# Kernel optimization log

Hardware: AMD Instinct MI355X
Metric: run time of the kernel (lower is better)

The kernel has to match this reference:

```python
import jax, jax.numpy as jnp
import numpy as np
from jax import lax

B, T, F, H, V, L = 64, 80, 4096, 512, 32000, 31


def _rn(k, shape, scale=0.05):
    return jax.random.normal(k, shape, dtype=jnp.float32) * scale


def setup_inputs() -> dict:
    key = jax.random.key(0)
    ks = jax.random.split(key, 16)
    emb = _rn(ks[0], (V, H)).at[0].set(0.0)  # padding_idx=0 row zeroed
    return dict(
        video_features=jax.random.normal(ks[1], (B, T, F), jnp.float32),
        captions=jax.random.randint(ks[2], (B, L), 0, V, jnp.int64),
        emb=emb,
        enc_Wih=_rn(ks[3], (4 * H, F)), enc_Whh=_rn(ks[4], (4 * H, H)),
        enc_bih=_rn(ks[5], (4 * H,)), enc_bhh=_rn(ks[6], (4 * H,)),
        attn_W=_rn(ks[7], (H, 2 * H)), attn_b=_rn(ks[8], (H,)),
        v_w=_rn(ks[9], (H,)),
        dec_Wih=_rn(ks[10], (4 * H, 2 * H)), dec_Whh=_rn(ks[11], (4 * H, H)),
        dec_bih=_rn(ks[12], (4 * H,)), dec_bhh=_rn(ks[13], (4 * H,)),
        fc_W=_rn(ks[14], (V, H)), fc_b=_rn(ks[15], (V,)),
    )


def _lstm_step(x, h, c, Wih, Whh, bih, bhh):
    # PyTorch gate order: i, f, g, o
    g = x @ Wih.T + bih + h @ Whh.T + bhh
    i, f, gg, o = jnp.split(g, 4, axis=-1)
    c = jax.nn.sigmoid(f) * c + jax.nn.sigmoid(i) * jnp.tanh(gg)
    h = jax.nn.sigmoid(o) * jnp.tanh(c)
    return h, c


def reference(video_features, captions, emb, enc_Wih, enc_Whh, enc_bih, enc_bhh,
              attn_W, attn_b, v_w, dec_Wih, dec_Whh, dec_bih, dec_bhh, fc_W, fc_b):
    b = video_features.shape[0]
    h_dim = enc_Whh.shape[1]
    h0 = jnp.zeros((b, h_dim), video_features.dtype)
    c0 = jnp.zeros((b, h_dim), video_features.dtype)

    # ---- encoder LSTM over time ----
    def enc_step(carry, x):
        h, c = carry
        h, c = _lstm_step(x, h, c, enc_Wih, enc_Whh, enc_bih, enc_bhh)
        return (h, c), h

    (h, c), enc_out = lax.scan(enc_step, (h0, c0), video_features.transpose(1, 0, 2))
    enc_out = enc_out.transpose(1, 0, 2)  # [B, T, H]

    # ---- attentive decoder, teacher forcing always on ----
    tokens = captions[:, :-1].T  # [L-1, B]

    def dec_step(carry, tok):
        h, c = carry
        e = emb[tok]  # [B, H]
        # Bahdanau attention: v . tanh(W [h; enc_out])
        hrep = jnp.broadcast_to(h[:, None, :], enc_out.shape)
        energy = jnp.tanh(jnp.concatenate([hrep, enc_out], axis=2) @ attn_W.T + attn_b)
        scores = energy @ v_w  # [B, T]
        w = jax.nn.softmax(scores, axis=1)
        ctx = jnp.einsum('bt,bth->bh', w, enc_out)
        x = jnp.concatenate([e, ctx], axis=1)  # [B, 2H]
        h, c = _lstm_step(x, h, c, dec_Wih, dec_Whh, dec_bih, dec_bhh)
        logits = h @ fc_W.T + fc_b  # [B, V]
        return (h, c), logits

    _, outs = lax.scan(dec_step, (h, c), tokens)
    return outs.transpose(1, 0, 2)  # [B, L-1, V]
```

## Files before the change

kernel.cpp:

```cpp
#include <hip/hip_runtime.h>


#define DEV __device__ __forceinline__

typedef __attribute__((ext_vector_type(4))) float f32x4;
typedef __attribute__((ext_vector_type(8))) short bf16x8;
typedef _Float16 half2_t __attribute__((ext_vector_type(2)));

static constexpr int B_ = 64, T_ = 80, H_ = 512, L_ = 31, NDEC = 30;

DEV unsigned short f2bf(float f) {
  unsigned u = __builtin_bit_cast(unsigned, f);
  u += 0x7FFF + ((u >> 16) & 1);
  return (unsigned short)(u >> 16);
}
DEV float bf2f(unsigned short s) {
  unsigned u = (unsigned)s << 16;
  return __builtin_bit_cast(float, u);
}
DEV unsigned short f2h(float x) { return __builtin_bit_cast(unsigned short, (_Float16)x); }
DEV float h2f(unsigned short h) { return (float)__builtin_bit_cast(_Float16, h); }
DEV unsigned f2h2(float lo, float hi) { return (unsigned)f2h(lo) | ((unsigned)f2h(hi) << 16); }
DEV float fdot2(unsigned x, unsigned w, float acc) {
  return __builtin_amdgcn_fdot2(__builtin_bit_cast(half2_t, x),
                                __builtin_bit_cast(half2_t, w), acc, false);
}
DEV float4 acc8(float4 a, uint4 hv, uint4 w0, uint4 w1, uint4 w2, uint4 w3) {
  a.x = fdot2(hv.x, w0.x, a.x); a.y = fdot2(hv.x, w0.y, a.y);
  a.z = fdot2(hv.x, w0.z, a.z); a.w = fdot2(hv.x, w0.w, a.w);
  a.x = fdot2(hv.y, w1.x, a.x); a.y = fdot2(hv.y, w1.y, a.y);
  a.z = fdot2(hv.y, w1.z, a.z); a.w = fdot2(hv.y, w1.w, a.w);
  a.x = fdot2(hv.z, w2.x, a.x); a.y = fdot2(hv.z, w2.y, a.y);
  a.z = fdot2(hv.z, w2.z, a.z); a.w = fdot2(hv.z, w2.w, a.w);
  a.x = fdot2(hv.w, w3.x, a.x); a.y = fdot2(hv.w, w3.y, a.y);
  a.z = fdot2(hv.w, w3.z, a.z); a.w = fdot2(hv.w, w3.w, a.w);
  return a;
}
DEV float accS(float s, uint4 hv, uint4 w) {
  s = fdot2(hv.x, w.x, s); s = fdot2(hv.y, w.y, s);
  s = fdot2(hv.z, w.z, s); s = fdot2(hv.w, w.w, s);
  return s;
}
DEV float sigmoidf(float x) { return 1.f / (1.f + __expf(-x)); }
DEV float tanh_fast(float x) { float e = __expf(2.f * x); return (e - 1.f) / (e + 1.f); }

DEV void astf(float* p, float v) { __hip_atomic_store(p, v, __ATOMIC_RELAXED, __HIP_MEMORY_SCOPE_AGENT); }
DEV void astu(unsigned* p, unsigned v) { __hip_atomic_store(p, v, __ATOMIC_RELAXED, __HIP_MEMORY_SCOPE_AGENT); }
DEV void asti(int* p, int v) { __hip_atomic_store(p, v, __ATOMIC_RELAXED, __HIP_MEMORY_SCOPE_AGENT); }
DEV float aldf(const float* p) { return __hip_atomic_load((float*)p, __ATOMIC_RELAXED, __HIP_MEMORY_SCOPE_AGENT); }
DEV unsigned aldu(const unsigned* p) { return __hip_atomic_load((unsigned*)p, __ATOMIC_RELAXED, __HIP_MEMORY_SCOPE_AGENT); }
DEV int aldi(const int* p) { return __hip_atomic_load((int*)p, __ATOMIC_RELAXED, __HIP_MEMORY_SCOPE_AGENT); }

DEV void tsync(int* tf, int m, int ph) {
  __syncthreads();
  if (threadIdx.x == 0) asti(tf + m * 16, ph);
  if (threadIdx.x < 4)
    while (aldi(tf + (int)threadIdx.x * 16) < ph) __builtin_amdgcn_s_sleep(1);
  __syncthreads();
}

__global__ __launch_bounds__(256) void k_cvt(const float* __restrict__ in,
                                             unsigned short* __restrict__ out, long n4) {
  long i = (long)blockIdx.x * 256 + threadIdx.x;
  long stride = (long)gridDim.x * 256;
  for (; i < n4; i += stride) {
    float4 v = reinterpret_cast<const float4*>(in)[i];
    ushort4 o;
    o.x = f2bf(v.x); o.y = f2bf(v.y); o.z = f2bf(v.z); o.w = f2bf(v.w);
    reinterpret_cast<ushort4*>(out)[i] = o;
  }
}

__global__ void k_detect_i64(const int* __restrict__ cap, int* __restrict__ flag) {
  __shared__ int s;
  if (threadIdx.x == 0) s = 0;
  __syncthreads();
  int acc = 0;
  for (int i = threadIdx.x; i < (B_ * L_) / 2; i += 256) acc |= cap[2 * i + 1];
  if (acc) atomicOr(&s, 1);
  __syncthreads();
  if (threadIdx.x == 0) flag[0] = (s == 0) ? 1 : 0;
}

__global__ __launch_bounds__(256) void k_gather_emb(const float* __restrict__ emb,
                                                    const int* __restrict__ cap,
                                                    const int* __restrict__ flag,
                                                    unsigned short* __restrict__ aemb) {
  int r = blockIdx.x;
  int l = r >> 6, b = r & 63;
  int ci = b * L_ + l;
  int tok = flag[0] ? cap[2 * ci] : cap[ci];
  const float* src = emb + (size_t)tok * H_;
  unsigned short* dst = aemb + (size_t)r * H_;
  for (int c = threadIdx.x; c < H_; c += 256) dst[c] = f2bf(src[c]);
}

__global__ __launch_bounds__(256) void k_pack_enc(const float* __restrict__ whh,
                                                  uint4* __restrict__ wpe) {
  int idx = blockIdx.x * 256 + threadIdx.x;
  int k2 = idx >> 9, j = idx & 511;
  float2 r0 = *(const float2*)(whh + (size_t)(j) * 512 + 2 * k2);
  float2 r1 = *(const float2*)(whh + (size_t)(512 + j) * 512 + 2 * k2);
  float2 r2 = *(const float2*)(whh + (size_t)(1024 + j) * 512 + 2 * k2);
  float2 r3 = *(const float2*)(whh + (size_t)(1536 + j) * 512 + 2 * k2);
  wpe[idx] = make_uint4(f2h2(r0.x, r0.y), f2h2(r1.x, r1.y), f2h2(r2.x, r2.y), f2h2(r3.x, r3.y));
}

__global__ __launch_bounds__(256) void k_pack_dec(const float* __restrict__ dwih,
                                                  const float* __restrict__ dwhh,
                                                  uint4* __restrict__ wpd) {
  int idx = blockIdx.x * 256 + threadIdx.x;
  int k2 = idx >> 9, j = idx & 511;
  float2 r[4];
  if (k2 < 256) {
#pragma unroll
    for (int g = 0; g < 4; ++g)
      r[g] = *(const float2*)(dwih + (size_t)(g * 512 + j) * 1024 + 512 + 2 * k2);
  } else {
#pragma unroll
    for (int g = 0; g < 4; ++g)
      r[g] = *(const float2*)(dwhh + (size_t)(g * 512 + j) * 512 + 2 * (k2 - 256));
  }
  wpd[idx] = make_uint4(f2h2(r[0].x, r[0].y), f2h2(r[1].x, r[1].y),
                        f2h2(r[2].x, r[2].y), f2h2(r[3].x, r[3].y));
}

__global__ __launch_bounds__(256) void k_pack_attn2(const float* __restrict__ attnw,
                                                    uint4* __restrict__ wat2) {
  int idx = blockIdx.x * 256 + threadIdx.x;
  int k8 = idx >> 9, u = idx & 511;
  const float* p = attnw + (size_t)u * 1024 + 8 * k8;
  wat2[idx] = make_uint4(f2h2(p[0], p[1]), f2h2(p[2], p[3]),
                         f2h2(p[4], p[5]), f2h2(p[6], p[7]));
}

template <int OUT_MODE>
__global__ __launch_bounds__(256) void k_gemm(const unsigned short* __restrict__ A, int lda,
                                              const unsigned short* __restrict__ Bm, int ldb,
                                              float* __restrict__ C, int N, int K,
                                              const float* __restrict__ bias0,
                                              const float* __restrict__ bias1) {
  __shared__ __align__(16) unsigned short As[128 * 40];
  __shared__ __align__(16) unsigned short Bs[128 * 40];
  const int tid = threadIdx.x;
  const int m0 = blockIdx.y * 128, n0 = blockIdx.x * 128;
  const int wave = tid >> 6, lane = tid & 63;
  const int wm = wave >> 1, wn = wave & 1;
  const int lr = lane & 15, lk = lane >> 4;

  f32x4 acc[4][4];
#pragma unroll
  for (int m = 0; m < 4; ++m)
#pragma unroll
    for (int n = 0; n < 4; ++n) acc[m][n] = (f32x4){0.f, 0.f, 0.f, 0.f};

  const int c0 = tid, c1 = tid + 256;
  const int ar0 = c0 >> 2, as0 = c0 & 3;
  const int ar1 = c1 >> 2, as1 = c1 & 3;

  for (int k0 = 0; k0 < K; k0 += 32) {
    uint4 va0 = *(const uint4*)(A + (size_t)(m0 + ar0) * lda + k0 + as0 * 8);
    uint4 va1 = *(const uint4*)(A + (size_t)(m0 + ar1) * lda + k0 + as1 * 8);
    uint4 vb0 = *(const uint4*)(Bm + (size_t)(n0 + ar0) * ldb + k0 + as0 * 8);
    uint4 vb1 = *(const uint4*)(Bm + (size_t)(n0 + ar1) * ldb + k0 + as1 * 8);
    *(uint4*)(As + ar0 * 40 + as0 * 8) = va0;
    *(uint4*)(As + ar1 * 40 + as1 * 8) = va1;
    *(uint4*)(Bs + ar0 * 40 + as0 * 8) = vb0;
    *(uint4*)(Bs + ar1 * 40 + as1 * 8) = vb1;
    __syncthreads();
    bf16x8 af[4], bfr[4];
#pragma unroll
    for (int m = 0; m < 4; ++m)
      af[m] = *(const bf16x8*)(As + (wm * 64 + m * 16 + lr) * 40 + lk * 8);
#pragma unroll
    for (int n = 0; n < 4; ++n)
      bfr[n] = *(const bf16x8*)(Bs + (wn * 64 + n * 16 + lr) * 40 + lk * 8);
#pragma unroll
    for (int m = 0; m < 4; ++m)
#pragma unroll
      for (int n = 0; n < 4; ++n)
        acc[m][n] = __builtin_amdgcn_mfma_f32_16x16x32_bf16(af[m], bfr[n], acc[m][n], 0, 0, 0);
    __syncthreads();
  }
#pragma unroll
  for (int m = 0; m < 4; ++m) {
#pragma unroll
    for (int n = 0; n < 4; ++n) {
      const int col = n0 + wn * 64 + n * 16 + lr;
      float bv = (bias0 ? bias0[col] : 0.f) + (bias1 ? bias1[col] : 0.f);
#pragma unroll
      for (int j = 0; j < 4; ++j) {
        const int row = m0 + wm * 64 + m * 16 + lk * 4 + j;
        float v = acc[m][n][j] + bv;
        if (OUT_MODE == 0) {
          C[(size_t)row * N + col] = v;
        } else if (OUT_MODE == 1) {
          int l = row >> 6, b = row & 63;
          C[((size_t)b * NDEC + l) * (size_t)N + col] = v;
        } else {
          C[((size_t)row * 512 + (col & 511)) * 4 + (col >> 9)] = v;
        }
      }
    }
  }
}

__global__ __launch_bounds__(1024) void k_enc4(const float4* __restrict__ xg4,
                                               const uint4* __restrict__ wpe,
                                               float* __restrict__ encf,
                                               unsigned short* __restrict__ encbf,
                                               float* __restrict__ cfin,
                                               unsigned* __restrict__ h16E,
                                               int* __restrict__ flagsE) {
  __shared__ __align__(16) unsigned short h16[512];
  __shared__ __align__(16) float psum[8 * 4 * 128];
  __shared__ unsigned short hnew[128];
  const int bid = blockIdx.x, b = bid >> 2, m = bid & 3, tid = threadIdx.x;
  const int j128 = tid & 127, ks = tid >> 7;
  const int j = m * 128 + j128;
  int* tf = flagsE + b * 64;
  float c = 0.f;
  if (tid < 256) ((unsigned*)h16)[tid] = 0u;
  __syncthreads();
  const uint4* hp4 = (const uint4*)h16;
  for (int t = 0; t < T_; ++t) {
    float4 a = {0.f, 0.f, 0.f, 0.f}, a1 = a;
#pragma unroll 2
    for (int k8 = ks * 8; k8 < ks * 8 + 8; k8 += 2) {
      uint4 h0 = hp4[k8], h1 = hp4[k8 + 1];
      a = acc8(a, h0, wpe[((k8 * 4 + 0) << 9) | j], wpe[((k8 * 4 + 1) << 9) | j],
               wpe[((k8 * 4 + 2) << 9) | j], wpe[((k8 * 4 + 3) << 9) | j]);
      a1 = acc8(a1, h1, wpe[((k8 * 4 + 4) << 9) | j], wpe[((k8 * 4 + 5) << 9) | j],
                wpe[((k8 * 4 + 6) << 9) | j], wpe[((k8 * 4 + 7) << 9) | j]);
    }
    psum[ks * 512 + 0 * 128 + j128] = a.x + a1.x;
    psum[ks * 512 + 1 * 128 + j128] = a.y + a1.y;
    psum[ks * 512 + 2 * 128 + j128] = a.z + a1.z;
    psum[ks * 512 + 3 * 128 + j128] = a.w + a1.w;
    __syncthreads();
    if (tid < 128) {
      float4 xa = xg4[((size_t)b * T_ + t) * 512 + m * 128 + tid];
      float g0 = xa.x, g1 = xa.y, g2 = xa.z, g3 = xa.w;
#pragma unroll
      for (int q = 0; q < 8; ++q) {
        g0 += psum[q * 512 + 0 * 128 + tid];
        g1 += psum[q * 512 + 1 * 128 + tid];
        g2 += psum[q * 512 + 2 * 128 + tid];
        g3 += psum[q * 512 + 3 * 128 + tid];
      }
      c = sigmoidf(g1) * c + sigmoidf(g0) * tanh_fast(g2);
      float h = sigmoidf(g3) * tanh_fast(c);
      size_t o = ((size_t)b * T_ + t) * 512 + m * 128 + tid;
      encf[o] = h;
      encbf[o] = f2bf(h);
      hnew[tid] = f2h(h);
      if (t == T_ - 1) cfin[b * 512 + m * 128 + tid] = c;
    }
    __syncthreads();
    const int p = t & 1;
    if (tid < 64)
      astu(h16E + (size_t)p * 64 * 256 + b * 256 + m * 64 + tid,
           (unsigned)hnew[2 * tid] | ((unsigned)hnew[2 * tid + 1] << 16));
    tsync(tf, m, t + 1);
    if (t < T_ - 1) {
      if (tid < 256)
        ((unsigned*)h16)[tid] = aldu(h16E + (size_t)p * 64 * 256 + b * 256 + tid);
      __syncthreads();
    }
  }
}

__global__ __launch_bounds__(1024) void k_dec4(const uint4* __restrict__ wpd,
                                               const uint4* __restrict__ wat2,
                                               const float* __restrict__ vw,
                                               const float4* __restrict__ eg4,
                                               const float* __restrict__ encpart,
                                               const unsigned short* __restrict__ encbf,
                                               const float* __restrict__ encf,
                                               const float* __restrict__ cfin,
                                               unsigned short* __restrict__ hsbf,
                                               float* __restrict__ hwbuf,
                                               float* __restrict__ scbuf,
                                               unsigned* __restrict__ ctxpH,
                                               unsigned* __restrict__ h16D,
                                               int* __restrict__ flagsD) {
  __shared__ __align__(16) unsigned short xv16[1024];
  __shared__ float hw[512];
  __shared__ float vsm[512];
  __shared__ float sc[80], wts[80];
  __shared__ __align__(16) float psum1[8 * 128];
  __shared__ __align__(16) float psum[8 * 4 * 128];
  __shared__ __align__(16) float4 ctxp[8 * 128];
  __shared__ unsigned short hnew[128];
  const int bid = blockIdx.x, b = bid >> 2, m = bid & 3, tid = threadIdx.x;
  int* tf = flagsD + b * 64;
  if (tid < 512) {
    vsm[tid] = vw[tid];
    xv16[512 + tid] = f2h(encf[((size_t)b * T_ + T_ - 1) * 512 + tid]);
  }
  float c = 0.f;
  if (tid < 128) c = cfin[b * 512 + m * 128 + tid];
  __syncthreads();
  const uint4* xp4 = (const uint4*)xv16;
  const uint4* xh4 = xp4 + 64;

  for (int l = 0; l < NDEC; ++l) {
    {
      const int u128 = tid & 127, ks = tid >> 7;
      const int u = m * 128 + u128;
      float s = 0.f, s1 = 0.f;
#pragma unroll 2
      for (int k8 = ks * 8; k8 < ks * 8 + 8; k8 += 2) {
        s = accS(s, xh4[k8], wat2[(k8 << 9) | u]);
        s1 = accS(s1, xh4[k8 + 1], wat2[((k8 + 1) << 9) | u]);
      }
      psum1[ks * 128 + u128] = s + s1;
    }
    __syncthreads();
    if (tid < 128) {
      float s = 0.f;
#pragma unroll
      for (int q = 0; q < 8; ++q) s += psum1[q * 128 + tid];
      astf(hwbuf + b * 512 + m * 128 + tid, s);
    }
    tsync(tf, m, 4 * l + 1);
    if (tid < 512) hw[tid] = aldf(hwbuf + b * 512 + tid);
    __syncthreads();
    {
      const int wv = tid >> 6, ln = tid & 63;
      for (int tt = wv; tt < 20; tt += 16) {
        const int t = m * 20 + tt;
        const float* ep = encpart + ((size_t)b * T_ + t) * 512;
        float p = 0.f;
#pragma unroll
        for (int q = 0; q < 8; ++q) {
          int u = ln + q * 64;
          p += vsm[u] * tanh_fast(hw[u] + ep[u]);
        }
#pragma unroll
        for (int s = 1; s < 64; s <<= 1) p += __shfl_xor(p, s, 64);
        if (ln == 0) astf(scbuf + b * 80 + t, p);
      }
    }
    tsync(tf, m, 4 * l + 2);
    if (tid < 80) sc[tid] = aldf(scbuf + b * 80 + tid);
    __syncthreads();
    if (tid < 64) {
      float x0 = sc[tid];
      float x1 = (tid < 16) ? sc[64 + tid] : -1e30f;
      float mx = fmaxf(x0, x1);
#pragma unroll
      for (int s = 1; s < 64; s <<= 1) mx = fmaxf(mx, __shfl_xor(mx, s, 64));
      float e0 = __expf(x0 - mx);
      float e1 = (tid < 16) ? __expf(x1 - mx) : 0.f;
      float sm = e0 + e1;
#pragma unroll
      for (int s = 1; s < 64; s <<= 1) sm += __shfl_xor(sm, s, 64);
      wts[tid] = e0 / sm;
      if (tid < 16) wts[64 + tid] = e1 / sm;
    }
    __syncthreads();
    {
      const int tsub = tid >> 7, j4 = tid & 127;
      float4 acc = {0.f, 0.f, 0.f, 0.f};
      for (int tl = tsub; tl < 20; tl += 8) {
        const int t = m * 20 + tl;
        float w = wts[t];
        ushort4 e = *(const ushort4*)(encbf + ((size_t)b * T_ + t) * 512 + j4 * 4);
        acc.x += w * bf2f(e.x); acc.y += w * bf2f(e.y);
        acc.z += w * bf2f(e.z); acc.w += w * bf2f(e.w);
      }
      ctxp[tsub * 128 + j4] = acc;
    }
    __syncthreads();
    if (tid < 256) {
      const float* cp = (const float*)ctxp;
      float s0 = 0.f, s1 = 0.f;
#pragma unroll
      for (int q = 0; q < 8; ++q) {
        s0 += cp[q * 512 + 2 * tid];
        s1 += cp[q * 512 + 2 * tid + 1];
      }
      astu(ctxpH + ((size_t)b * 4 + m) * 256 + tid, f2h2(s0, s1));
    }
    tsync(tf, m, 4 * l + 3);
    if (tid < 256) {
      float s0 = 0.f, s1 = 0.f;
#pragma unroll
      for (int mm = 0; mm < 4; ++mm) {
        unsigned u = aldu(ctxpH + ((size_t)b * 4 + mm) * 256 + tid);
        s0 += h2f((unsigned short)(u & 0xffffu));
        s1 += h2f((unsigned short)(u >> 16));
      }
      ((unsigned*)xv16)[tid] = f2h2(s0, s1);
    }
    __syncthreads();
    {
      const int j128 = tid & 127, ks = tid >> 7;
      const int j = m * 128 + j128;
      float4 a = {0.f, 0.f, 0.f, 0.f}, a1 = a;
#pragma unroll 2
      for (int k8 = ks * 16; k8 < ks * 16 + 16; k8 += 2) {
        uint4 h0 = xp4[k8], h1 = xp4[k8 + 1];
        a = acc8(a, h0, wpd[((k8 * 4 + 0) << 9) | j], wpd[((k8 * 4 + 1) << 9) | j],
                 wpd[((k8 * 4 + 2) << 9) | j], wpd[((k8 * 4 + 3) << 9) | j]);
        a1 = acc8(a1, h1, wpd[((k8 * 4 + 4) << 9) | j], wpd[((k8 * 4 + 5) << 9) | j],
                  wpd[((k8 * 4 + 6) << 9) | j], wpd[((k8 * 4 + 7) << 9) | j]);
      }
      psum[ks * 512 + 0 * 128 + j128] = a.x + a1.x;
      psum[ks * 512 + 1 * 128 + j128] = a.y + a1.y;
      psum[ks * 512 + 2 * 128 + j128] = a.z + a1.z;
      psum[ks * 512 + 3 * 128 + j128] = a.w + a1.w;
    }
    __syncthreads();
    if (tid < 128) {
      float4 xa = eg4[((size_t)l * 64 + b) * 512 + m * 128 + tid];
      float g0 = xa.x, g1 = xa.y, g2 = xa.z, g3 = xa.w;
#pragma unroll
      for (int q = 0; q < 8; ++q) {
        g0 += psum[q * 512 + 0 * 128 + tid];
        g1 += psum[q * 512 + 1 * 128 + tid];
        g2 += psum[q * 512 + 2 * 128 + tid];
        g3 += psum[q * 512 + 3 * 128 + tid];
      }
      c = sigmoidf(g1) * c + sigmoidf(g0) * tanh_fast(g2);
      float h = sigmoidf(g3) * tanh_fast(c);
      hsbf[((size_t)l * 64 + b) * 512 + m * 128 + tid] = f2bf(h);
      hnew[tid] = f2h(h);
    }
    __syncthreads();
    const int p = l & 1;
    if (tid < 64)
      astu(h16D + (size_t)p * 64 * 256 + b * 256 + m * 64 + tid,
           (unsigned)hnew[2 * tid] | ((unsigned)hnew[2 * tid + 1] << 16));
    tsync(tf, m, 4 * l + 4);
    if (l < NDEC - 1) {
      if (tid < 256)
        ((unsigned*)xv16)[256 + tid] = aldu(h16D + (size_t)p * 64 * 256 + b * 256 + tid);
      __syncthreads();
    }
  }
}

extern "C" void kernel_launch(void* const* d_in, const int* in_sizes, int n_in,
                              void* d_out, int out_size, void* d_ws, size_t ws_size,
                              hipStream_t stream) {
  const float* video = (const float*)d_in[0];
  const int* captions = (const int*)d_in[1];
  const float* emb = (const float*)d_in[2];
  const float* eWih = (const float*)d_in[3];
  const float* eWhh = (const float*)d_in[4];
  const float* ebih = (const float*)d_in[5];
  const float* ebhh = (const float*)d_in[6];
  const float* attnW = (const float*)d_in[7];
  const float* attnb = (const float*)d_in[8];
  const float* vw = (const float*)d_in[9];
  const float* dWih = (const float*)d_in[10];
  const float* dWhh = (const float*)d_in[11];
  const float* dbih = (const float*)d_in[12];
  const float* dbhh = (const float*)d_in[13];
  const float* fcW = (const float*)d_in[14];
  const float* fcb = (const float*)d_in[15];

  char* ws = (char*)d_ws;
  unsigned short* vid_bf = (unsigned short*)(ws + 0);
  unsigned short* fcw_bf = (unsigned short*)(ws + 0);
  const size_t G = 32768000ull;
  unsigned* h16E = (unsigned*)(ws + G + 0);
  unsigned* h16D = (unsigned*)(ws + G + 131072);
  float* hwbufD = (float*)(ws + G + 262144);
  float* scbufD = (float*)(ws + G + 393216);
  unsigned* ctxpH = (unsigned*)(ws + G + 413696);
  int* flagsE = (int*)(ws + G + 675840);
  int* flagsD = (int*)(ws + G + 692224);
  unsigned short* hs_bf = (unsigned short*)(ws + 33554432ull);
  uint4* wpd = (uint4*)(ws + 35520512ull);
  uint4* wpe = (uint4*)(ws + 39714816ull);
  float* xg4 = (float*)(ws + 41943040ull);
  float* encpart = (float*)(ws + 41943040ull);
  float* eg4 = (float*)(ws + 52428800ull);
  unsigned short* aemb = (unsigned short*)(ws + 68157440ull);
  unsigned short* ewih_bf = (unsigned short*)(ws + 83886080ull);
  float* encf = (float*)(ws + 100663296ull);
  unsigned short* encbf = (unsigned short*)(ws + 111149056ull);
  unsigned short* attnw_bf = (unsigned short*)(ws + 116391936ull);
  unsigned short* dwih_bf = (unsigned short*)(ws + 117440512ull);
  uint4* wat2 = (uint4*)(ws + 121634816ull);
  float* cfin = (float*)(ws + 122159104ull);
  int* flag = (int*)(ws + 122290176ull);

  auto cvt = [&](const float* in, unsigned short* out, long n) {
    long n4 = n / 4;
    int blocks = (int)((n4 + 255) / 256);
    if (blocks > 2048) blocks = 2048;
    k_cvt<<<blocks, 256, 0, stream>>>(in, out, n4);
  };
  cvt(video, vid_bf, 5120L * 4096);
  cvt(eWih, ewih_bf, 2048L * 4096);
  cvt(attnW, attnw_bf, 512L * 1024);
  cvt(dWih, dwih_bf, 2048L * 1024);
  k_detect_i64<<<1, 256, 0, stream>>>(captions, flag);

  k_gemm<2><<<dim3(16, 40), 256, 0, stream>>>(vid_bf, 4096, ewih_bf, 4096, xg4, 2048, 4096, ebih, ebhh);
  cvt(fcW, fcw_bf, 32000L * 512);

  k_pack_enc<<<512, 256, 0, stream>>>(eWhh, wpe);
  k_pack_dec<<<1024, 256, 0, stream>>>(dWih, dWhh, wpd);
  k_pack_attn2<<<128, 256, 0, stream>>>(attnW, wat2);

  hipMemsetAsync(ws + G + 675840, 0, 32768, stream);

  k_enc4<<<256, 1024, 0, stream>>>((const float4*)xg4, wpe, encf, encbf, cfin, h16E, flagsE);

  k_gather_emb<<<1920, 256, 0, stream>>>(emb, captions, flag, aemb);
  k_gemm<0><<<dim3(4, 40), 256, 0, stream>>>(encbf, 512, attnw_bf + 512, 1024, encpart, 512, 512, attnb, nullptr);
  k_gemm<2><<<dim3(16, 15), 256, 0, stream>>>(aemb, 512, dwih_bf, 1024, eg4, 2048, 512, dbih, dbhh);

  k_dec4<<<256, 1024, 0, stream>>>(wpd, wat2, vw, (const float4*)eg4, encpart, encbf, encf,
                                   cfin, hs_bf, hwbufD, scbufD, ctxpH, h16D, flagsD);

  k_gemm<1><<<dim3(250, 15), 256, 0, stream>>>(hs_bf, 512, fcw_bf, 512, (float*)d_out, 32000, 512, fcb, nullptr);
}
```

Measured before the change: 1.389 ms.

## Cut decoder cross-block syncs from four to two per step; prefetch GEMM tiles

In the decoder, each of the four blocks working on one batch row now computes partial attention scores over all 80 timesteps using only its own 128 hidden units of the attention projection. It publishes those partial scores, and the partials are summed after a single tile sync. This drops the separate exchange of the projected hidden state. The context vector is now computed redundantly in every block over all timesteps, so the ctx-partial exchange and its sync are also removed, leaving two flag syncs per step instead of four. Separately, the GEMM loads the next K-slice of global data into registers before the MFMA work, overlapping memory latency with compute at the cost of more registers.

```diff
diff --git a/kernel.cpp b/kernel.cpp
--- a/kernel.cpp
+++ b/kernel.cpp
@@ -157,17 +157,28 @@
   const int c0 = tid, c1 = tid + 256;
   const int ar0 = c0 >> 2, as0 = c0 & 3;
   const int ar1 = c1 >> 2, as1 = c1 & 3;
+  const unsigned short* pa0 = A + (size_t)(m0 + ar0) * lda + as0 * 8;
+  const unsigned short* pa1 = A + (size_t)(m0 + ar1) * lda + as1 * 8;
+  const unsigned short* pb0 = Bm + (size_t)(n0 + ar0) * ldb + as0 * 8;
+  const unsigned short* pb1 = Bm + (size_t)(n0 + ar1) * ldb + as1 * 8;
+
+  uint4 va0 = *(const uint4*)(pa0);
+  uint4 va1 = *(const uint4*)(pa1);
+  uint4 vb0 = *(const uint4*)(pb0);
+  uint4 vb1 = *(const uint4*)(pb1);
 
   for (int k0 = 0; k0 < K; k0 += 32) {
-    uint4 va0 = *(const uint4*)(A + (size_t)(m0 + ar0) * lda + k0 + as0 * 8);
-    uint4 va1 = *(const uint4*)(A + (size_t)(m0 + ar1) * lda + k0 + as1 * 8);
-    uint4 vb0 = *(const uint4*)(Bm + (size_t)(n0 + ar0) * ldb + k0 + as0 * 8);
-    uint4 vb1 = *(const uint4*)(Bm + (size_t)(n0 + ar1) * ldb + k0 + as1 * 8);
     *(uint4*)(As + ar0 * 40 + as0 * 8) = va0;
     *(uint4*)(As + ar1 * 40 + as1 * 8) = va1;
     *(uint4*)(Bs + ar0 * 40 + as0 * 8) = vb0;
     *(uint4*)(Bs + ar1 * 40 + as1 * 8) = vb1;
     __syncthreads();
+    if (k0 + 32 < K) {
+      va0 = *(const uint4*)(pa0 + k0 + 32);
+      va1 = *(const uint4*)(pa1 + k0 + 32);
+      vb0 = *(const uint4*)(pb0 + k0 + 32);
+      vb1 = *(const uint4*)(pb1 + k0 + 32);
+    }
     bf16x8 af[4], bfr[4];
 #pragma unroll
     for (int m = 0; m < 4; ++m)
@@ -270,7 +281,7 @@
   }
 }
 
-__global__ __launch_bounds__(1024) void k_dec4(const uint4* __restrict__ wpd,
+__global__ __launch_bounds__(1024) void k_dec5(const uint4* __restrict__ wpd,
                                                const uint4* __restrict__ wat2,
                                                const float* __restrict__ vw,
                                                const float4* __restrict__ eg4,
@@ -279,18 +290,16 @@
                                                const float* __restrict__ encf,
                                                const float* __restrict__ cfin,
                                                unsigned short* __restrict__ hsbf,
-                                               float* __restrict__ hwbuf,
-                                               float* __restrict__ scbuf,
-                                               unsigned* __restrict__ ctxpH,
+                                               float* __restrict__ scpart,
                                                unsigned* __restrict__ h16D,
                                                int* __restrict__ flagsD) {
   __shared__ __align__(16) unsigned short xv16[1024];
-  __shared__ float hw[512];
   __shared__ float vsm[512];
+  __shared__ float hwOwn[128];
   __shared__ float sc[80], wts[80];
   __shared__ __align__(16) float psum1[8 * 128];
   __shared__ __align__(16) float psum[8 * 4 * 128];
-  __shared__ __align__(16) float4 ctxp[8 * 128];
+  __shared__ __align__(16) float ctxp[4 * 512];
   __shared__ unsigned short hnew[128];
   const int bid = blockIdx.x, b = bid >> 2, m = bid & 3, tid = threadIdx.x;
   int* tf = flagsD + b * 64;
@@ -321,29 +330,27 @@
       float s = 0.f;
 #pragma unroll
       for (int q = 0; q < 8; ++q) s += psum1[q * 128 + tid];
-      astf(hwbuf + b * 512 + m * 128 + tid, s);
-    }
-    tsync(tf, m, 4 * l + 1);
-    if (tid < 512) hw[tid] = aldf(hwbuf + b * 512 + tid);
+      hwOwn[tid] = s;
+    }
     __syncthreads();
     {
       const int wv = tid >> 6, ln = tid & 63;
-      for (int tt = wv; tt < 20; tt += 16) {
-        const int t = m * 20 + tt;
-        const float* ep = encpart + ((size_t)b * T_ + t) * 512;
-        float p = 0.f;
-#pragma unroll
-        for (int q = 0; q < 8; ++q) {
-          int u = ln + q * 64;
-          p += vsm[u] * tanh_fast(hw[u] + ep[u]);
-        }
+      for (int t = wv; t < T_; t += 16) {
+        const float* ep = encpart + ((size_t)b * T_ + t) * 512 + m * 128;
+        float p = vsm[m * 128 + ln] * tanh_fast(hwOwn[ln] + ep[ln]) +
+                  vsm[m * 128 + 64 + ln] * tanh_fast(hwOwn[64 + ln] + ep[64 + ln]);
 #pragma unroll
         for (int s = 1; s < 64; s <<= 1) p += __shfl_xor(p, s, 64);
-        if (ln == 0) astf(scbuf + b * 80 + t, p);
-      }
-    }
-    tsync(tf, m, 4 * l + 2);
-    if (tid < 80) sc[tid] = aldf(scbuf + b * 80 + tid);
+        if (ln == 0) astf(scpart + ((size_t)b * 4 + m) * 80 + t, p);
+      }
+    }
+    tsync(tf, m, 2 * l + 1);
+    if (tid < 80) {
+      float s = 0.f;
+#pragma unroll
+      for (int mm = 0; mm < 4; ++mm) s += aldf(scpart + ((size_t)b * 4 + mm) * 80 + tid);
+      sc[tid] = s;
+    }
     __syncthreads();
     if (tid < 64) {
       float x0 = sc[tid];
@@ -361,36 +368,24 @@
     }
     __syncthreads();
     {
-      const int tsub = tid >> 7, j4 = tid & 127;
-      float4 acc = {0.f, 0.f, 0.f, 0.f};
-      for (int tl = tsub; tl < 20; tl += 8) {
-        const int t = m * 20 + tl;
+      const int j2 = tid & 255, tsub = tid >> 8;
+      float a0 = 0.f, a1 = 0.f;
+      for (int t = tsub; t < T_; t += 4) {
         float w = wts[t];
-        ushort4 e = *(const ushort4*)(encbf + ((size_t)b * T_ + t) * 512 + j4 * 4);
-        acc.x += w * bf2f(e.x); acc.y += w * bf2f(e.y);
-        acc.z += w * bf2f(e.z); acc.w += w * bf2f(e.w);
-      }
-      ctxp[tsub * 128 + j4] = acc;
-    }
-    __syncthreads();
-    if (tid < 256) {
-      const float* cp = (const float*)ctxp;
-      float s0 = 0.f, s1 = 0.f;
-#pragma unroll
-      for (int q = 0; q < 8; ++q) {
-        s0 += cp[q * 512 + 2 * tid];
-        s1 += cp[q * 512 + 2 * tid + 1];
-      }
-      astu(ctxpH + ((size_t)b * 4 + m) * 256 + tid, f2h2(s0, s1));
-    }
-    tsync(tf, m, 4 * l + 3);
+        unsigned e = *(const unsigned*)(encbf + ((size_t)b * T_ + t) * 512 + 2 * j2);
+        a0 += w * bf2f((unsigned short)(e & 0xffffu));
+        a1 += w * bf2f((unsigned short)(e >> 16));
+      }
+      ctxp[tsub * 512 + 2 * j2] = a0;
+      ctxp[tsub * 512 + 2 * j2 + 1] = a1;
+    }
+    __syncthreads();
     if (tid < 256) {
       float s0 = 0.f, s1 = 0.f;
 #pragma unroll
-      for (int mm = 0; mm < 4; ++mm) {
-        unsigned u = aldu(ctxpH + ((size_t)b * 4 + mm) * 256 + tid);
-        s0 += h2f((unsigned short)(u & 0xffffu));
-        s1 += h2f((unsigned short)(u >> 16));
+      for (int q = 0; q < 4; ++q) {
+        s0 += ctxp[q * 512 + 2 * tid];
+        s1 += ctxp[q * 512 + 2 * tid + 1];
       }
       ((unsigned*)xv16)[tid] = f2h2(s0, s1);
     }
@@ -433,7 +428,7 @@
     if (tid < 64)
       astu(h16D + (size_t)p * 64 * 256 + b * 256 + m * 64 + tid,
            (unsigned)hnew[2 * tid] | ((unsigned)hnew[2 * tid + 1] << 16));
-    tsync(tf, m, 4 * l + 4);
+    tsync(tf, m, 2 * l + 2);
     if (l < NDEC - 1) {
       if (tid < 256)
         ((unsigned*)xv16)[256 + tid] = aldu(h16D + (size_t)p * 64 * 256 + b * 256 + tid);
@@ -468,9 +463,7 @@
   const size_t G = 32768000ull;
   unsigned* h16E = (unsigned*)(ws + G + 0);
   unsigned* h16D = (unsigned*)(ws + G + 131072);
-  float* hwbufD = (float*)(ws + G + 262144);
-  float* scbufD = (float*)(ws + G + 393216);
-  unsigned* ctxpH = (unsigned*)(ws + G + 413696);
+  float* scpartD = (float*)(ws + G + 262144);
   int* flagsE = (int*)(ws + G + 675840);
   int* flagsD = (int*)(ws + G + 692224);
   unsigned short* hs_bf = (unsigned short*)(ws + 33554432ull);
@@ -516,8 +509,8 @@
   k_gemm<0><<<dim3(4, 40), 256, 0, stream>>>(encbf, 512, attnw_bf + 512, 1024, encpart, 512, 512, attnb, nullptr);
   k_gemm<2><<<dim3(16, 15), 256, 0, stream>>>(aemb, 512, dwih_bf, 1024, eg4, 2048, 512, dbih, dbhh);
 
-  k_dec4<<<256, 1024, 0, stream>>>(wpd, wat2, vw, (const float4*)eg4, encpart, encbf, encf,
-                                   cfin, hs_bf, hwbufD, scbufD, ctxpH, h16D, flagsD);
+  k_dec5<<<256, 1024, 0, stream>>>(wpd, wat2, vw, (const float4*)eg4, encpart, encbf, encf,
+                                   cfin, hs_bf, scpartD, h16D, flagsD);
 
   k_gemm<1><<<dim3(250, 15), 256, 0, stream>>>(hs_bf, 512, fcw_bf, 512, (float*)d_out, 32000, 512, fcb, nullptr);
 }
```

Result: slower. 1.586 ms (+14.2%).
